# Kernel optimization log

Hardware: AMD Instinct MI355X
Metric: run time of the kernel (lower is better)

Reference implementation:

```python
import jax, jax.numpy as jnp
import numpy as np

N_NODES = 50000
N_EDGES = 800000
IN_DIM = 128
HID_DIM = 64
OUT_DIM = 64
NUM_GRAPHS = 512


def setup_inputs() -> dict:
    key = jax.random.key(0)
    ks = jax.random.split(key, 8)
    x = jax.random.normal(ks[0], (N_NODES, IN_DIM), dtype=jnp.float32)
    edge_index = jax.random.randint(ks[1], (2, N_EDGES), 0, N_NODES, dtype=jnp.int64)
    batch = jnp.sort(jax.random.randint(ks[2], (N_NODES,), 0, NUM_GRAPHS, dtype=jnp.int64))
    s1 = 1.0 / np.sqrt(IN_DIM)
    s2 = 1.0 / np.sqrt(HID_DIM)
    W1 = jax.random.uniform(ks[3], (IN_DIM, HID_DIM), jnp.float32, -s1, s1)
    b1 = jax.random.uniform(ks[4], (HID_DIM,), jnp.float32, -s1, s1)
    W2 = jax.random.uniform(ks[5], (HID_DIM, OUT_DIM), jnp.float32, -s2, s2)
    b2 = jax.random.uniform(ks[6], (OUT_DIM,), jnp.float32, -s2, s2)
    return {"x": x, "edge_index": edge_index, "batch": batch,
            "W1": W1, "b1": b1, "W2": W2, "b2": b2}


def _gcn_layer(h, W, b, src, dst, norm, n_nodes):
    # linear transform first (keeps the per-edge gather at output width)
    h = h @ W + b                      # [N, d_out]
    msg = h[src] * norm[:, None]       # [E, d_out] gathered, normalized messages
    agg = jax.ops.segment_sum(msg, dst, num_segments=n_nodes)  # scatter-add
    return jax.nn.relu(agg)


def reference(x, edge_index, batch, W1, b1, W2, b2):
    src, dst = edge_index[0], edge_index[1]
    # symmetric degree normalization: deg^{-1/2}[src] * deg^{-1/2}[dst]
    deg = jax.ops.segment_sum(jnp.ones((src.shape[0],), x.dtype), dst,
                              num_segments=N_NODES)
    dinv = jax.lax.rsqrt(jnp.maximum(deg, 1.0))
    norm = dinv[src] * dinv[dst]       # [E]

    h = _gcn_layer(x, W1, b1, src, dst, norm, N_NODES)   # dropout = identity (eval)
    h = _gcn_layer(h, W2, b2, src, dst, norm, N_NODES)

    # scatter_mean pooling over batch indices
    sums = jax.ops.segment_sum(h, batch, num_segments=NUM_GRAPHS)
    cnts = jax.ops.segment_sum(jnp.ones((N_NODES,), h.dtype), batch,
                               num_segments=NUM_GRAPHS)
    return sums / jnp.maximum(cnts, 1.0)[:, None]        # [NUM_GRAPHS, OUT_DIM]
```

## Files before the change

kernel.cpp:

```cpp
#include <hip/hip_runtime.h>
#include <hip/hip_fp16.h>

#define N_NODES 50000
#define N_EDGES 800000
#define IN_DIM 128
#define NUM_GRAPHS 512
#define CAP 64
#define NB 392
#define BCAP 2816
#define FILL_T 2048
#define NFILL 391
#define GEMM1_BLKS 391
#define GEMM_TILES 1563

typedef unsigned short u16;
typedef unsigned int u32;

__device__ __forceinline__ void acc_row(const uint4& v, float2& aa, float2& ab,
                                        float2& ac, float2& ad) {
    const __half2* hp = reinterpret_cast<const __half2*>(&v);
    float2 f;
    f = __half22float2(hp[0]); aa.x += f.x; aa.y += f.y;
    f = __half22float2(hp[1]); ab.x += f.x; ab.y += f.y;
    f = __half22float2(hp[2]); ac.x += f.x; ac.y += f.y;
    f = __half22float2(hp[3]); ad.x += f.x; ad.y += f.y;
}

__device__ __forceinline__ void acc_row_s(const uint4& v, float dv, float2& aa,
                                          float2& ab, float2& ac, float2& ad) {
    const __half2* hp = reinterpret_cast<const __half2*>(&v);
    float2 f;
    f = __half22float2(hp[0]); aa.x = fmaf(f.x, dv, aa.x); aa.y = fmaf(f.y, dv, aa.y);
    f = __half22float2(hp[1]); ab.x = fmaf(f.x, dv, ab.x); ab.y = fmaf(f.y, dv, ab.y);
    f = __half22float2(hp[2]); ac.x = fmaf(f.x, dv, ac.x); ac.y = fmaf(f.y, dv, ac.y);
    f = __half22float2(hp[3]); ad.x = fmaf(f.x, dv, ad.x); ad.y = fmaf(f.y, dv, ad.y);
}

__device__ __forceinline__ void gather_node(
    const uint4* __restrict__ H16, const u16* __restrict__ sp, int dg, int lo,
    float2& aa, float2& ab, float2& ac, float2& ad) {
    int i = 0;
    for (; i + 7 < dg; i += 8) {
        ushort4 s4a = *reinterpret_cast<const ushort4*>(sp + i);
        ushort4 s4b = *reinterpret_cast<const ushort4*>(sp + i + 4);
        uint4 v0 = H16[(size_t)s4a.x * 8 + lo];
        uint4 v1 = H16[(size_t)s4a.y * 8 + lo];
        uint4 v2 = H16[(size_t)s4a.z * 8 + lo];
        uint4 v3 = H16[(size_t)s4a.w * 8 + lo];
        uint4 v4 = H16[(size_t)s4b.x * 8 + lo];
        uint4 v5 = H16[(size_t)s4b.y * 8 + lo];
        uint4 v6 = H16[(size_t)s4b.z * 8 + lo];
        uint4 v7 = H16[(size_t)s4b.w * 8 + lo];
        acc_row(v0, aa, ab, ac, ad); acc_row(v1, aa, ab, ac, ad);
        acc_row(v2, aa, ab, ac, ad); acc_row(v3, aa, ab, ac, ad);
        acc_row(v4, aa, ab, ac, ad); acc_row(v5, aa, ab, ac, ad);
        acc_row(v6, aa, ab, ac, ad); acc_row(v7, aa, ab, ac, ad);
    }
    for (; i + 3 < dg; i += 4) {
        ushort4 s4 = *reinterpret_cast<const ushort4*>(sp + i);
        uint4 v0 = H16[(size_t)s4.x * 8 + lo];
        uint4 v1 = H16[(size_t)s4.y * 8 + lo];
        uint4 v2 = H16[(size_t)s4.z * 8 + lo];
        uint4 v3 = H16[(size_t)s4.w * 8 + lo];
        acc_row(v0, aa, ab, ac, ad); acc_row(v1, aa, ab, ac, ad);
        acc_row(v2, aa, ab, ac, ad); acc_row(v3, aa, ab, ac, ad);
    }
    for (; i < dg; ++i) {
        uint4 v = H16[(size_t)sp[i] * 8 + lo];
        acc_row(v, aa, ab, ac, ad);
    }
}

__device__ __forceinline__ void gather_node_s(
    const uint4* __restrict__ H16, const u16* __restrict__ sp,
    const float* __restrict__ dinv, int dg, int lo,
    float2& aa, float2& ab, float2& ac, float2& ad) {
    int i = 0;
    for (; i + 7 < dg; i += 8) {
        ushort4 s4a = *reinterpret_cast<const ushort4*>(sp + i);
        ushort4 s4b = *reinterpret_cast<const ushort4*>(sp + i + 4);
        uint4 v0 = H16[(size_t)s4a.x * 8 + lo];
        uint4 v1 = H16[(size_t)s4a.y * 8 + lo];
        uint4 v2 = H16[(size_t)s4a.z * 8 + lo];
        uint4 v3 = H16[(size_t)s4a.w * 8 + lo];
        uint4 v4 = H16[(size_t)s4b.x * 8 + lo];
        uint4 v5 = H16[(size_t)s4b.y * 8 + lo];
        uint4 v6 = H16[(size_t)s4b.z * 8 + lo];
        uint4 v7 = H16[(size_t)s4b.w * 8 + lo];
        float d0 = dinv[s4a.x], d1 = dinv[s4a.y], d2 = dinv[s4a.z], d3 = dinv[s4a.w];
        float d4 = dinv[s4b.x], d5 = dinv[s4b.y], d6 = dinv[s4b.z], d7 = dinv[s4b.w];
        acc_row_s(v0, d0, aa, ab, ac, ad); acc_row_s(v1, d1, aa, ab, ac, ad);
        acc_row_s(v2, d2, aa, ab, ac, ad); acc_row_s(v3, d3, aa, ab, ac, ad);
        acc_row_s(v4, d4, aa, ab, ac, ad); acc_row_s(v5, d5, aa, ab, ac, ad);
        acc_row_s(v6, d6, aa, ab, ac, ad); acc_row_s(v7, d7, aa, ab, ac, ad);
    }
    for (; i + 3 < dg; i += 4) {
        ushort4 s4 = *reinterpret_cast<const ushort4*>(sp + i);
        uint4 v0 = H16[(size_t)s4.x * 8 + lo];
        uint4 v1 = H16[(size_t)s4.y * 8 + lo];
        uint4 v2 = H16[(size_t)s4.z * 8 + lo];
        uint4 v3 = H16[(size_t)s4.w * 8 + lo];
        float d0 = dinv[s4.x], d1 = dinv[s4.y], d2 = dinv[s4.z], d3 = dinv[s4.w];
        acc_row_s(v0, d0, aa, ab, ac, ad); acc_row_s(v1, d1, aa, ab, ac, ad);
        acc_row_s(v2, d2, aa, ab, ac, ad); acc_row_s(v3, d3, aa, ab, ac, ad);
    }
    for (; i < dg; ++i) {
        uint4 v = H16[(size_t)sp[i] * 8 + lo];
        float dv = dinv[sp[i]];
        acc_row_s(v, dv, aa, ab, ac, ad);
    }
}

__global__ __launch_bounds__(256) void gemm1_fill_kernel(
    const float* __restrict__ X, const float* __restrict__ W,
    const float* __restrict__ bias, __half* __restrict__ Yh, int n_nodes,
    const int* __restrict__ src, const int* __restrict__ dst,
    int* __restrict__ gcursor, u32* __restrict__ packed, int n_edges) {
    __shared__ float xst[32][128];
    __shared__ float ws[32][64];
    __shared__ int cnt2[NB], goffs[NB];
    const int tid = threadIdx.x;

    if (blockIdx.x & 1) {
        const int fb = blockIdx.x >> 1;
        for (int i = tid; i < NB; i += 256) cnt2[i] = 0;
        __syncthreads();
        const int base = fb * FILL_T;
        int d[8], s[8], pl[8];
#pragma unroll
        for (int i = 0; i < 8; ++i) {
            int e = base + i * 256 + tid;
            if (e < n_edges) {
                d[i] = dst[e]; s[i] = src[e];
                pl[i] = atomicAdd(&cnt2[d[i] >> 7], 1);
            } else d[i] = -1;
        }
        __syncthreads();
        for (int b = tid; b < NB; b += 256)
            if (cnt2[b] > 0) goffs[b] = atomicAdd(&gcursor[b], cnt2[b]);
        __syncthreads();
#pragma unroll
        for (int i = 0; i < 8; ++i) {
            if (d[i] >= 0) {
                int b = d[i] >> 7;
                packed[(size_t)b * BCAP + goffs[b] + pl[i]] =
                    ((u32)d[i] << 16) | (u32)s[i];
            }
        }
        return;
    }

    const int idx = blockIdx.x >> 1;
    if (idx >= GEMM1_BLKS) return;
    const int base = idx * 128;
    const int lane = tid & 63;
    const int w = tid >> 6;
    const int jo = lane & 7;
    const int rg = lane >> 3;
    const int rowb = w * 32 + rg * 4;

    float cc[4][8];
    {
        float4 ba = *reinterpret_cast<const float4*>(bias + jo * 8);
        float4 bb = *reinterpret_cast<const float4*>(bias + jo * 8 + 4);
#pragma unroll
        for (int r = 0; r < 4; ++r) {
            cc[r][0] = ba.x; cc[r][1] = ba.y; cc[r][2] = ba.z; cc[r][3] = ba.w;
            cc[r][4] = bb.x; cc[r][5] = bb.y; cc[r][6] = bb.z; cc[r][7] = bb.w;
        }
    }
    const float4* X4 = reinterpret_cast<const float4*>(X);
    const float4* W4 = reinterpret_cast<const float4*>(W);
    float4* ws4 = reinterpret_cast<float4*>(&ws[0][0]);

    for (int kc = 0; kc < 4; ++kc) {
        if (kc) __syncthreads();
#pragma unroll
        for (int t = 0; t < 4; ++t) {
            int i = t * 256 + tid;
            int row = i >> 3, f4 = i & 7;
            float4 v = make_float4(0.f, 0.f, 0.f, 0.f);
            if (base + row < n_nodes) v = X4[(size_t)(base + row) * 32 + kc * 8 + f4];
            int k0 = f4 * 4;
            xst[k0 + 0][row] = v.x; xst[k0 + 1][row] = v.y;
            xst[k0 + 2][row] = v.z; xst[k0 + 3][row] = v.w;
        }
#pragma unroll
        for (int t = 0; t < 2; ++t)
            ws4[t * 256 + tid] = W4[kc * 512 + t * 256 + tid];
        __syncthreads();

#pragma unroll 8
        for (int kk = 0; kk < 32; ++kk) {
            float4 xv = *reinterpret_cast<const float4*>(&xst[kk][rowb]);
            float4 wa = *reinterpret_cast<const float4*>(&ws[kk][jo * 8]);
            float4 wb = *reinterpret_cast<const float4*>(&ws[kk][jo * 8 + 4]);
            float xr[4] = {xv.x, xv.y, xv.z, xv.w};
            float wv[8] = {wa.x, wa.y, wa.z, wa.w, wb.x, wb.y, wb.z, wb.w};
#pragma unroll
            for (int r = 0; r < 4; ++r)
#pragma unroll
                for (int j = 0; j < 8; ++j) cc[r][j] += xr[r] * wv[j];
        }
    }

#pragma unroll
    for (int r = 0; r < 4; ++r) {
        int row = base + rowb + r;
        if (row < n_nodes) {
            __half2 h0 = __floats2half2_rn(cc[r][0], cc[r][1]);
            __half2 h1 = __floats2half2_rn(cc[r][2], cc[r][3]);
            __half2 h2 = __floats2half2_rn(cc[r][4], cc[r][5]);
            __half2 h3 = __floats2half2_rn(cc[r][6], cc[r][7]);
            uint4 o;
            o.x = *reinterpret_cast<u32*>(&h0); o.y = *reinterpret_cast<u32*>(&h1);
            o.z = *reinterpret_cast<u32*>(&h2); o.w = *reinterpret_cast<u32*>(&h3);
            *reinterpret_cast<uint4*>(Yh + (size_t)row * 64 + jo * 8) = o;
        }
    }
}

__global__ __launch_bounds__(256) void fine_kernel(
    const u32* __restrict__ packed, const int* __restrict__ gcursor,
    u16* __restrict__ ssorted, int* __restrict__ deg, float* __restrict__ dinv,
    const int* __restrict__ batch, int* __restrict__ gstart, int n_graphs) {
    __shared__ u16 image[128 * CAP];
    __shared__ int cur[128];
    const int tid = threadIdx.x;

    if (blockIdx.x == NB) {
        for (int g = tid; g <= n_graphs; g += 256) {
            int lo = 0, hi = N_NODES;
            while (lo < hi) {
                int mid = (lo + hi) >> 1;
                if (batch[mid] < g) lo = mid + 1; else hi = mid;
            }
            gstart[g] = lo;
        }
        return;
    }

    const int b = blockIdx.x;
    if (tid < 128) cur[tid] = 0;
    __syncthreads();
    const int cnt = gcursor[b];
    const u32* pp = packed + (size_t)b * BCAP;
    for (int i = tid; i < cnt; i += 256) {
        u32 p = pp[i];
        int loc = (p >> 16) & 127;
        int pos = atomicAdd(&cur[loc], 1);
        if (pos < CAP) image[loc * CAP + pos] = (u16)(p & 0xffff);
    }
    __syncthreads();
    const int nbase = b * 128;
    if (tid < 128) {
        int c = cur[tid];
        int d = nbase + tid;
        if (d < N_NODES) {
            deg[d] = c;
            dinv[d] = rsqrtf(fmaxf((float)c, 1.0f));
        }
    }
    __syncthreads();
    const u32* im32 = reinterpret_cast<const u32*>(image);
    u32* out32 = reinterpret_cast<u32*>(ssorted) + (size_t)nbase * (CAP / 2);
    for (int i = tid; i < 128 * CAP / 2; i += 256) out32[i] = im32[i];
}

__global__ __launch_bounds__(256) void agg_gemm_kernel(
    const __half* __restrict__ H, const u16* __restrict__ ssorted,
    const int* __restrict__ deg, const float* __restrict__ dinv,
    const float* __restrict__ W, const float* __restrict__ bias,
    __half* __restrict__ Yh, int n_nodes) {
    __shared__ float xs[32][64];
    const int tid = threadIdx.x;
    const int lane = tid & 63;
    const int w = tid >> 6;
    const int lo = lane & 7;
    const int slot = w * 8 + (lane >> 3);
    const int base = blockIdx.x * 32;
    const uint4* H16 = reinterpret_cast<const uint4*>(H);

    int node = base + slot;
    float2 aa = make_float2(0.f, 0.f), ab = make_float2(0.f, 0.f);
    float2 ac = make_float2(0.f, 0.f), ad = make_float2(0.f, 0.f);
    if (node < n_nodes) {
        int dg = min(deg[node], CAP);
        gather_node_s(H16, ssorted + (size_t)node * CAP, dinv, dg, lo, aa, ab, ac, ad);
        float dv = dinv[node];
        *reinterpret_cast<float4*>(&xs[slot][8 * lo]) =
            make_float4(fmaxf(aa.x * dv, 0.f), fmaxf(aa.y * dv, 0.f),
                        fmaxf(ab.x * dv, 0.f), fmaxf(ab.y * dv, 0.f));
        *reinterpret_cast<float4*>(&xs[slot][8 * lo + 4]) =
            make_float4(fmaxf(ac.x * dv, 0.f), fmaxf(ac.y * dv, 0.f),
                        fmaxf(ad.x * dv, 0.f), fmaxf(ad.y * dv, 0.f));
    } else {
        *reinterpret_cast<float4*>(&xs[slot][8 * lo]) = make_float4(0.f, 0.f, 0.f, 0.f);
        *reinterpret_cast<float4*>(&xs[slot][8 * lo + 4]) = make_float4(0.f, 0.f, 0.f, 0.f);
    }
    __syncthreads();

    float b = bias[lane];
    float c[8];
#pragma unroll
    for (int r = 0; r < 8; ++r) c[r] = b;
#pragma unroll 4
    for (int k = 0; k < 64; ++k) {
        float wv = W[k * 64 + lane];
#pragma unroll
        for (int r = 0; r < 8; ++r) c[r] += wv * xs[w * 8 + r][k];
    }
    int n0 = base + w * 8;
#pragma unroll
    for (int r = 0; r < 8; ++r)
        if (n0 + r < n_nodes)
            Yh[(size_t)(n0 + r) * 64 + lane] = __float2half(c[r] * dinv[n0 + r]);
}

__global__ __launch_bounds__(512) void agg2_pool_kernel(
    const __half* __restrict__ H, const u16* __restrict__ ssorted,
    const int* __restrict__ deg, const float* __restrict__ dinv,
    const int* __restrict__ gstart, float* __restrict__ out) {
    __shared__ float part[64][64];
    const int g = blockIdx.x;
    const int tid = threadIdx.x;
    const int lane = tid & 63;
    const int w = tid >> 6;
    const int lo = lane & 7;
    const int slot = w * 8 + (lane >> 3);
    const uint4* H16 = reinterpret_cast<const uint4*>(H);
    const int beg = gstart[g], end = gstart[g + 1];

    float2 pa = make_float2(0.f, 0.f), pb = make_float2(0.f, 0.f);
    float2 pc = make_float2(0.f, 0.f), pd = make_float2(0.f, 0.f);
    for (int node = beg + slot; node < end; node += 64) {
        int dg = min(deg[node], CAP);
        float2 aa = make_float2(0.f, 0.f), ab = make_float2(0.f, 0.f);
        float2 ac = make_float2(0.f, 0.f), ad = make_float2(0.f, 0.f);
        gather_node(H16, ssorted + (size_t)node * CAP, dg, lo, aa, ab, ac, ad);
        float dv = dinv[node];
        pa.x += fmaxf(aa.x * dv, 0.f); pa.y += fmaxf(aa.y * dv, 0.f);
        pb.x += fmaxf(ab.x * dv, 0.f); pb.y += fmaxf(ab.y * dv, 0.f);
        pc.x += fmaxf(ac.x * dv, 0.f); pc.y += fmaxf(ac.y * dv, 0.f);
        pd.x += fmaxf(ad.x * dv, 0.f); pd.y += fmaxf(ad.y * dv, 0.f);
    }
    *reinterpret_cast<float4*>(&part[slot][8 * lo]) = make_float4(pa.x, pa.y, pb.x, pb.y);
    *reinterpret_cast<float4*>(&part[slot][8 * lo + 4]) = make_float4(pc.x, pc.y, pd.x, pd.y);
    __syncthreads();
    if (tid < 64) {
        float s = 0.f;
#pragma unroll
        for (int r = 0; r < 64; ++r) s += part[r][tid];
        out[(size_t)g * 64 + tid] = s / fmaxf((float)(end - beg), 1.0f);
    }
}

extern "C" void kernel_launch(void* const* d_in, const int* in_sizes, int n_in,
                              void* d_out, int out_size, void* d_ws, size_t ws_size,
                              hipStream_t stream) {
    const float* x     = (const float*)d_in[0];
    const int*   ei    = (const int*)d_in[1];
    const int*   batch = (const int*)d_in[2];
    const float* W1    = (const float*)d_in[3];
    const float* b1    = (const float*)d_in[4];
    const float* W2    = (const float*)d_in[5];
    const float* b2    = (const float*)d_in[6];
    float* out = (float*)d_out;

    const int* srcp = ei;
    const int* dstp = ei + N_EDGES;

    __half* H1h     = (__half*)d_ws;
    __half* H2h     = H1h + (size_t)N_NODES * 64;
    float*  dinv    = (float*)(H2h + (size_t)N_NODES * 64);
    int*    deg     = (int*)(dinv + N_NODES);
    u16*    ssorted = (u16*)(deg + N_NODES);
    u32*    packed  = (u32*)(ssorted + (size_t)NB * 128 * CAP);
    int*    gcursor = (int*)(packed + (size_t)NB * BCAP);
    int*    gstart  = gcursor + NB;

    hipMemsetAsync(gcursor, 0, NB * sizeof(int), stream);

    gemm1_fill_kernel<<<2 * NFILL, 256, 0, stream>>>(
        x, W1, b1, H1h, N_NODES, srcp, dstp, gcursor, packed, N_EDGES);

    fine_kernel<<<NB + 1, 256, 0, stream>>>(
        packed, gcursor, ssorted, deg, dinv, batch, gstart, NUM_GRAPHS);

    agg_gemm_kernel<<<GEMM_TILES, 256, 0, stream>>>(
        H1h, ssorted, deg, dinv, W2, b2, H2h, N_NODES);

    agg2_pool_kernel<<<NUM_GRAPHS, 512, 0, stream>>>(
        H2h, ssorted, deg, dinv, gstart, out);
}
```

Baseline: 170.7 us.

## Enlarge agg_gemm tile to 128 nodes with register-blocked GEMM and shared W

Each agg_gemm block now gathers and aggregates 128 nodes (four passes of 32) instead of 32, and stages W2 in shared memory once per block. The small GEMM becomes a register-blocked 8x4 outer-product tile per thread using float4 LDS reads from a padded xs array, and the output is written as packed half4 stores. This aims to cut redundant global W loads and LDS traffic per FMA. The trade-off is fewer blocks (391), more LDS per block, and more registers, which may reduce occupancy and latency hiding during the gather phase.

```diff
diff --git a/kernel.cpp b/kernel.cpp
--- a/kernel.cpp
+++ b/kernel.cpp
@@ -11,7 +11,7 @@
 #define FILL_T 2048
 #define NFILL 391
 #define GEMM1_BLKS 391
-#define GEMM_TILES 1563
+#define AGG_BLKS 391
 
 typedef unsigned short u16;
 typedef unsigned int u32;
@@ -272,49 +272,91 @@
     const int* __restrict__ deg, const float* __restrict__ dinv,
     const float* __restrict__ W, const float* __restrict__ bias,
     __half* __restrict__ Yh, int n_nodes) {
-    __shared__ float xs[32][64];
+    __shared__ float xs[128][68];
+    __shared__ float ws[64][64];
     const int tid = threadIdx.x;
     const int lane = tid & 63;
     const int w = tid >> 6;
     const int lo = lane & 7;
-    const int slot = w * 8 + (lane >> 3);
-    const int base = blockIdx.x * 32;
+    const int grp = tid >> 3;
+    const int base = blockIdx.x * 128;
     const uint4* H16 = reinterpret_cast<const uint4*>(H);
 
-    int node = base + slot;
-    float2 aa = make_float2(0.f, 0.f), ab = make_float2(0.f, 0.f);
-    float2 ac = make_float2(0.f, 0.f), ad = make_float2(0.f, 0.f);
-    if (node < n_nodes) {
-        int dg = min(deg[node], CAP);
-        gather_node_s(H16, ssorted + (size_t)node * CAP, dinv, dg, lo, aa, ab, ac, ad);
-        float dv = dinv[node];
+    {
+        const float4* W4 = reinterpret_cast<const float4*>(W);
+        float4* ws4 = reinterpret_cast<float4*>(&ws[0][0]);
+#pragma unroll
+        for (int t = 0; t < 4; ++t) ws4[t * 256 + tid] = W4[t * 256 + tid];
+    }
+
+    for (int t = 0; t < 4; ++t) {
+        int slot = grp + 32 * t;
+        int node = base + slot;
+        float2 aa = make_float2(0.f, 0.f), ab = make_float2(0.f, 0.f);
+        float2 ac = make_float2(0.f, 0.f), ad = make_float2(0.f, 0.f);
+        float dv = 0.f;
+        if (node < n_nodes) {
+            int dg = min(deg[node], CAP);
+            gather_node_s(H16, ssorted + (size_t)node * CAP, dinv, dg, lo,
+                          aa, ab, ac, ad);
+            dv = dinv[node];
+        }
         *reinterpret_cast<float4*>(&xs[slot][8 * lo]) =
             make_float4(fmaxf(aa.x * dv, 0.f), fmaxf(aa.y * dv, 0.f),
                         fmaxf(ab.x * dv, 0.f), fmaxf(ab.y * dv, 0.f));
         *reinterpret_cast<float4*>(&xs[slot][8 * lo + 4]) =
             make_float4(fmaxf(ac.x * dv, 0.f), fmaxf(ac.y * dv, 0.f),
                         fmaxf(ad.x * dv, 0.f), fmaxf(ad.y * dv, 0.f));
-    } else {
-        *reinterpret_cast<float4*>(&xs[slot][8 * lo]) = make_float4(0.f, 0.f, 0.f, 0.f);
-        *reinterpret_cast<float4*>(&xs[slot][8 * lo + 4]) = make_float4(0.f, 0.f, 0.f, 0.f);
     }
     __syncthreads();
 
-    float b = bias[lane];
-    float c[8];
-#pragma unroll
-    for (int r = 0; r < 8; ++r) c[r] = b;
+    const int half = w >> 1;
+    const int rg = lane >> 3;
+    const int c0 = (w & 1) * 32 + lo * 4;
+    float cc[8][4];
+    {
+        float4 bv = *reinterpret_cast<const float4*>(bias + c0);
+#pragma unroll
+        for (int i = 0; i < 8; ++i) {
+            cc[i][0] = bv.x; cc[i][1] = bv.y; cc[i][2] = bv.z; cc[i][3] = bv.w;
+        }
+    }
 #pragma unroll 4
-    for (int k = 0; k < 64; ++k) {
-        float wv = W[k * 64 + lane];
-#pragma unroll
-        for (int r = 0; r < 8; ++r) c[r] += wv * xs[w * 8 + r][k];
-    }
-    int n0 = base + w * 8;
-#pragma unroll
-    for (int r = 0; r < 8; ++r)
-        if (n0 + r < n_nodes)
-            Yh[(size_t)(n0 + r) * 64 + lane] = __float2half(c[r] * dinv[n0 + r]);
+    for (int k = 0; k < 64; k += 4) {
+        float4 xv[8];
+#pragma unroll
+        for (int i = 0; i < 8; ++i)
+            xv[i] = *reinterpret_cast<const float4*>(&xs[half * 64 + rg + 8 * i][k]);
+        float wr[4][4];
+#pragma unroll
+        for (int j = 0; j < 4; ++j) {
+            float4 wv = *reinterpret_cast<const float4*>(&ws[k + j][c0]);
+            wr[j][0] = wv.x; wr[j][1] = wv.y; wr[j][2] = wv.z; wr[j][3] = wv.w;
+        }
+#pragma unroll
+        for (int i = 0; i < 8; ++i) {
+            float xr[4] = {xv[i].x, xv[i].y, xv[i].z, xv[i].w};
+#pragma unroll
+            for (int kk = 0; kk < 4; ++kk)
+#pragma unroll
+                for (int j = 0; j < 4; ++j)
+                    cc[i][j] = fmaf(xr[kk], wr[kk][j], cc[i][j]);
+        }
+    }
+
+#pragma unroll
+    for (int i = 0; i < 8; ++i) {
+        int row = base + half * 64 + rg + 8 * i;
+        if (row < n_nodes) {
+            float dv = dinv[row];
+            __half2 h0 = __floats2half2_rn(cc[i][0] * dv, cc[i][1] * dv);
+            __half2 h1 = __floats2half2_rn(cc[i][2] * dv, cc[i][3] * dv);
+            uint2 o;
+            o.x = *reinterpret_cast<u32*>(&h0);
+            o.y = *reinterpret_cast<u32*>(&h1);
+            *reinterpret_cast<uint2*>(Yh + (size_t)row * 64 + c0) = o;
+        }
+    }
 }
 
 __global__ __launch_bounds__(512) void agg2_pool_kernel(
@@ -387,7 +429,7 @@
     fine_kernel<<<NB + 1, 256, 0, stream>>>(
         packed, gcursor, ssorted, deg, dinv, batch, gstart, NUM_GRAPHS);
 
-    agg_gemm_kernel<<<GEMM_TILES, 256, 0, stream>>>(
+    agg_gemm_kernel<<<AGG_BLKS, 256, 0, stream>>>(
         H1h, ssorted, deg, dinv, W2, b2, H2h, N_NODES);
 
     agg2_pool_kernel<<<NUM_GRAPHS, 512, 0, stream>>>(
```

Measured after the change: 172.9 us. Within noise of the previous version (+1.3%).
